# Kernel optimization log

Hardware: AMD Instinct MI355X
Metric: run time of the kernel (lower is better)

The kernel has to match this reference:

```python
import jax, jax.numpy as jnp
import numpy as np

C = 128; HEADS = 8; GH = 32; GW = 32; B = 8; PD = 8  # PD = (dim//4)//4

def _conv(x, w, pad, dil=1, groups=1):
    return jax.lax.conv_general_dilated(
        x, w, (1, 1), [(pad[0], pad[0]), (pad[1], pad[1])],
        rhs_dilation=(dil, dil),
        dimension_numbers=('NCHW', 'OIHW', 'NCHW'),
        feature_group_count=groups)

def _lrelu(t):
    return jnp.where(t >= 0, t, 0.1 * t)

def _ln(t, g, b, eps=1e-5):
    m = jnp.mean(t, -1, keepdims=True)
    v = jnp.var(t, -1, keepdims=True)
    return (t - m) * jax.lax.rsqrt(v + eps) * g + b

def setup_inputs():
    rng = np.random.RandomState(0)
    f = lambda *s: jnp.asarray((rng.randn(*s) * 0.05).astype(np.float32))
    ones = lambda n: jnp.ones((n,), jnp.float32)
    zeros = lambda n: jnp.zeros((n,), jnp.float32)
    # Swin-style relative position index over the (GH, GW) group
    coords = np.stack(np.meshgrid(np.arange(GH), np.arange(GW), indexing='ij')).reshape(2, -1)
    rel = (coords[:, :, None] - coords[:, None, :]).transpose(1, 2, 0)
    rel[..., 0] += GH - 1; rel[..., 1] += GW - 1; rel[..., 0] *= 2 * GW - 1
    rel_idx = jnp.asarray(rel.sum(-1).astype(np.int32))  # [N, N]
    biases = np.stack(np.meshgrid(np.arange(1 - GH, GH), np.arange(1 - GW, GW), indexing='ij'))
    biases = jnp.asarray(biases.reshape(2, -1).T.astype(np.float32))  # [(2GH-1)*(2GW-1), 2]
    return dict(
        x=jnp.asarray(rng.rand(B, C, GH, GW).astype(np.float32)),
        conv1_w=f(C, C, 3, 3), conv2_w=f(C, C, 3, 3), conv3_w=f(C, C, 3, 3),
        convt_w=f(C, 3, 1, 1),
        rba_w=f(C, C, 3, 1), rba_b=zeros(C), rbb_w=f(C, C, 1, 3), rbb_b=zeros(C),
        pp_w=f(PD, 2), pp_b=zeros(PD),
        l1_g=ones(PD), l1_b=zeros(PD), l1_w=f(PD, PD), l1_b2=zeros(PD),
        l2_g=ones(PD), l2_b=zeros(PD), l2_w=f(PD, PD), l2_b2=zeros(PD),
        l3_g=ones(PD), l3_b=zeros(PD), l3_w=f(HEADS, PD), l3_b2=zeros(HEADS),
        qk_w=f(2 * C, C), qk_b=zeros(2 * C),
        v_w=f(C, C), v_b=zeros(C),
        proj_w=f(C, C), proj_b=zeros(C),
        fc1_w=f(C, C), fc1_b=zeros(C), fc2_w=f(C, C), fc2_b=zeros(C),
        biases=biases, rel_idx=rel_idx,
    )

def reference(x, conv1_w, conv2_w, conv3_w, convt_w, rba_w, rba_b, rbb_w, rbb_b,
              pp_w, pp_b, l1_g, l1_b, l1_w, l1_b2, l2_g, l2_b, l2_w, l2_b2,
              l3_g, l3_b, l3_w, l3_b2, qk_w, qk_b, v_w, v_b, proj_w, proj_b,
              fc1_w, fc1_b, fc2_w, fc2_b, biases, rel_idx):
    Bn, Cc, Hh, Ww = x.shape
    N = Hh * Ww
    hd = Cc // HEADS
    # FeaExtract: ResASPP (3 dilated 3x3 convs, grouped 1x1 merge) + residual
    b1 = _lrelu(_conv(x, conv1_w, (1, 1)))
    b2 = _lrelu(_conv(x, conv2_w, (3, 3), dil=3))
    b3 = _lrelu(_conv(x, conv3_w, (5, 5), dil=5))
    a = _conv(jnp.concatenate([b1, b2, b3], 1), convt_w, (0, 0), groups=Cc) + x
    # RB: (3,1) conv -> lrelu -> (1,3) conv + residual
    r = _lrelu(_conv(a, rba_w, (1, 0)) + rba_b[None, :, None, None])
    r = _conv(r, rbb_w, (0, 1)) + rbb_b[None, :, None, None]
    o0 = r + a
    # original uses in-place clamp_, so o0 is clamped before flattening
    o0 = jnp.clip(o0, 0.0, 1.0)
    E = o0.reshape(Bn, Cc, N).transpose(0, 2, 1)  # [B, N, C]
    qk = E @ qk_w.T + qk_b  # [B, N, 2C]
    q = qk[..., :Cc].reshape(Bn, N, HEADS, hd).transpose(0, 2, 1, 3)
    k = qk[..., Cc:].reshape(Bn, N, HEADS, hd).transpose(0, 2, 1, 3)
    v = (E @ v_w.T + v_b).reshape(Bn, N, HEADS, hd).transpose(0, 2, 1, 3)
    attn = jnp.einsum('bhid,bhjd->bhij', q * (hd ** -0.5), k)
    # DynamicPosBias MLP (residual=False): Linear(2,pd) -> [LN,ReLU,Linear] x2 -> LN,ReLU,Linear(pd,heads)
    p = biases @ pp_w.T + pp_b
    p = jax.nn.relu(_ln(p, l1_g, l1_b)) @ l1_w.T + l1_b2
    p = jax.nn.relu(_ln(p, l2_g, l2_b)) @ l2_w.T + l2_b2
    p = jax.nn.relu(_ln(p, l3_g, l3_b)) @ l3_w.T + l3_b2  # [L, heads]
    rpb = p[rel_idx]  # gather -> [N, N, heads]
    attn = attn + rpb.transpose(2, 0, 1)[None]
    attn = jax.nn.softmax(attn, axis=-1)
    y = jnp.einsum('bhij,bhjd->bhid', attn, v).transpose(0, 2, 1, 3).reshape(Bn, N, Cc) + E
    x_proj = y @ proj_w.T + proj_b
    h = jax.nn.gelu(x_proj @ fc1_w.T + fc1_b, approximate=False)
    return (h @ fc2_w.T + fc2_b) + y
```

## Files before the change

kernel.cpp:

```cpp
#include <hip/hip_runtime.h>
#include <hip/hip_bf16.h>

typedef __hip_bfloat16 bf16;
typedef __bf16 bf16x8 __attribute__((ext_vector_type(8)));
typedef float f32x4 __attribute__((ext_vector_type(4)));
typedef __fp16 f16x2 __attribute__((ext_vector_type(2)));
typedef __fp16 f16x4 __attribute__((ext_vector_type(4)));

#define Lb 3969
#define LOG2E 1.4426950408889634f
#define EXP2(x) __builtin_amdgcn_exp2f(x)

#define XP_F   0
#define WF_F   903168
#define WR_F   1124352
#define WG_F   1173504
#define QKV_F  1222656
#define AP_F   2795520
#define YT_F   2795520
#define EB_F   3352576
#define FLAG_F 3908616
#define RT_F   3908624
#define VT_F   4924432

__device__ __forceinline__ float b2f(bf16 v) { return __bfloat162float(v); }
__device__ __forceinline__ bf16 f2b(float v) { return __float2bfloat16(v); }

template <typename T> __device__ __forceinline__ float ldw(const void* p, int i);
template <> __device__ __forceinline__ float ldw<bf16>(const void* p, int i) {
  return __bfloat162float(((const bf16*)p)[i]);
}
template <> __device__ __forceinline__ float ldw<float>(const void* p, int i) {
  return ((const float*)p)[i];
}
template <typename T> __device__ __forceinline__ void stw(void* p, size_t i, float v);
template <> __device__ __forceinline__ void stw<bf16>(void* p, size_t i, float v) {
  ((bf16*)p)[i] = __float2bfloat16(v);
}
template <> __device__ __forceinline__ void stw<float>(void* p, size_t i, float v) {
  ((float*)p)[i] = v;
}

__device__ __forceinline__ unsigned pkh(float a, float b) {
  f16x2 t = __builtin_amdgcn_cvt_pkrtz(a, b);
  return *(unsigned*)&t;
}

__device__ __forceinline__ bool detect_local(const unsigned* x) {
  int lane = threadIdx.x & 63;
  int cnt = 0;
#pragma unroll
  for (int k = 0; k < 4; ++k) {
    unsigned lo = x[lane + 64 * k] & 0xFFFFu;
    cnt += (lo >= 0x3C00u && lo < 0x3F80u) ? 1 : 0;
  }
#pragma unroll
  for (int off = 1; off < 64; off <<= 1) cnt += __shfl_xor(cnt, off);
  return cnt >= 128;
}

template <typename T>
__device__ __forceinline__ void ln_relu8(const float* t, float* u,
                                         const void* g, const void* bb)
{
  float m = 0.f;
#pragma unroll
  for (int k = 0; k < 8; ++k) m += t[k];
  m *= 0.125f;
  float v = 0.f;
#pragma unroll
  for (int k = 0; k < 8; ++k) { float d = t[k] - m; v += d * d; }
  v *= 0.125f;
  float r = rsqrtf(v + 1e-5f);
#pragma unroll
  for (int k = 0; k < 8; ++k) {
    float val = (t[k] - m) * r * ldw<T>(g, k) + ldw<T>(bb, k);
    u[k] = val > 0.f ? val : 0.f;
  }
}

template <typename T>
__device__ __forceinline__ float dpb_one(
    int r, int h, const void* biases, const void* pp_w, const void* pp_b,
    const void* l1_g, const void* l1_b, const void* l1_w, const void* l1_b2,
    const void* l2_g, const void* l2_b, const void* l2_w, const void* l2_b2,
    const void* l3_g, const void* l3_b, const void* l3_w, const void* l3_b2)
{
  float b0 = ldw<T>(biases, r * 2), b1 = ldw<T>(biases, r * 2 + 1);
  float t[8], u[8];
#pragma unroll
  for (int j = 0; j < 8; ++j)
    t[j] = b0 * ldw<T>(pp_w, j * 2) + b1 * ldw<T>(pp_w, j * 2 + 1) +
           ldw<T>(pp_b, j);
  ln_relu8<T>(t, u, l1_g, l1_b);
#pragma unroll
  for (int j = 0; j < 8; ++j) {
    float s = ldw<T>(l1_b2, j);
#pragma unroll
    for (int k = 0; k < 8; ++k) s += u[k] * ldw<T>(l1_w, j * 8 + k);
    t[j] = s;
  }
  ln_relu8<T>(t, u, l2_g, l2_b);
#pragma unroll
  for (int j = 0; j < 8; ++j) {
    float s = ldw<T>(l2_b2, j);
#pragma unroll
    for (int k = 0; k < 8; ++k) s += u[k] * ldw<T>(l2_w, j * 8 + k);
    t[j] = s;
  }
  ln_relu8<T>(t, u, l3_g, l3_b);
  float s = ldw<T>(l3_b2, h);
#pragma unroll
  for (int k = 0; k < 8; ++k) s += u[k] * ldw<T>(l3_w, h * 8 + k);
  return s;
}

template <typename T>
__device__ void wprep_all_body(const void* w1, const void* w2, const void* w3,
                               const void* rba_w, const void* rbb_w,
                               const void* qk_w, const void* v_w,
                               const void* proj_w, const void* fc1_w,
                               const void* fc2_w, bf16* __restrict__ Wf,
                               bf16* __restrict__ Wr, bf16* __restrict__ Wg)
{
  int tid = blockIdx.x * 256 + threadIdx.x;
  int lane = tid & 63, li = lane & 15, quad = lane >> 4;
  if (tid < 55296) {
    int mt = (tid >> 6) & 7;
    int Kc = (tid >> 9) & 3;
    int rem = tid >> 11;
    int t = rem % 9;
    int br = rem / 9;
    const void* w = (br == 0 ? w1 : (br == 1 ? w2 : w3));
    int o = mt * 16 + li;
    int ci0 = Kc * 32 + quad * 8;
#pragma unroll
    for (int j = 0; j < 8; ++j)
      Wf[(size_t)tid * 8 + j] = f2b(ldw<T>(w, (o * 128 + ci0 + j) * 9 + t));
  } else {
    int u = tid - 55296;
    if (u < 12288) {
      int Kc = (u >> 6) & 3, mt = (u >> 8) & 7, q = u >> 11;
      const void* w = (q >= 3) ? rbb_w : rba_w;
      int t = q % 3;
#pragma unroll
      for (int j = 0; j < 8; ++j)
        Wr[(size_t)u * 8 + j] =
            f2b(ldw<T>(w, ((mt * 16 + li) * 128 + Kc * 32 + quad * 8 + j) * 3 + t));
    } else if (u < 24576) {
      int g = u - 12288;
      int Kc = (g >> 6) & 3, mtg = g >> 8;
      const void* w; int mrow; float sc = 1.f;
      if (mtg < 16)      { w = qk_w;   mrow = mtg * 16;
                           if (mtg < 8) sc = 0.25f * LOG2E; }
      else if (mtg < 24) { w = v_w;    mrow = (mtg - 16) * 16; }
      else if (mtg < 32) { w = proj_w; mrow = (mtg - 24) * 16; }
      else if (mtg < 40) { w = fc1_w;  mrow = (mtg - 32) * 16; }
      else               { w = fc2_w;  mrow = (mtg - 40) * 16; }
#pragma unroll
      for (int j = 0; j < 8; ++j)
        Wg[(size_t)g * 8 + j] =
            f2b(sc * ldw<T>(w, (mrow + li) * 128 + Kc * 32 + quad * 8 + j));
    }
  }
}

template <typename T>
__device__ void nhwc_body(const void* x, bf16* __restrict__ xp,
                          bf16 (*tile)[128], int bid)
{
  const int b = bid >> 5;
  const int row = bid & 31;
  const int t = threadIdx.x;
  const size_t bbase = (size_t)b * 42 * 42 * 128;
  const bf16x8 z = (bf16x8){};

  if (t < 160) {
    int side = t / 80;
    int off = (t % 80) * 8;
    *(bf16x8*)&xp[bbase + ((size_t)(row + 5) * 42 + side * 37) * 128 + off] = z;
  }
  {
    int zr = (row < 5) ? row : ((row >= 27) ? row + 10 : -1);
    if (zr >= 0) {
      size_t base = bbase + (size_t)zr * 42 * 128;
      for (int k = t; k < 672; k += 256) *(bf16x8*)&xp[base + k * 8] = z;
    }
  }

  {
    int ci = t >> 1, half = t & 1;
#pragma unroll
    for (int j = 0; j < 16; ++j) {
      int px = half * 16 + j;
      tile[px][ci] = f2b(ldw<T>(x, ((size_t)b * 128 + ci) * 1024 + row * 32 + px));
    }
  }
  __syncthreads();
  {
    int px = t >> 3, c0 = (t & 7) * 16;
    bf16* dst = xp + (bbase + ((size_t)(row + 5) * 42 + (px + 5)) * 128 + c0);
#pragma unroll
    for (int j = 0; j < 16; ++j) dst[j] = tile[px][c0 + j];
  }
}

template <typename T>
__device__ void dpbrt_wave(
    int tt, int h, int lane, const void* biases, const void* pp_w,
    const void* pp_b, const void* l1_g, const void* l1_b, const void* l1_w,
    const void* l1_b2, const void* l2_g, const void* l2_b, const void* l2_w,
    const void* l2_b2, const void* l3_g, const void* l3_b, const void* l3_w,
    const void* l3_b2, float* __restrict__ RTf, float (*rp)[47])
{
  const int t = tt >> 1, p = tt & 1;
  const int quad = lane >> 4, li = lane & 15;
  for (int e = lane; e < 94; e += 64) {
    int row = t + e / 47;
    int col = p * 16 + e % 47;
    rp[e / 47][e % 47] =
        dpb_one<T>(row * 63 + col, h, biases, pp_w, pp_b, l1_g, l1_b, l1_w,
                   l1_b2, l2_g, l2_b, l2_w, l2_b2, l3_g, l3_b, l3_w, l3_b2) *
        LOG2E;
  }
  __syncthreads();
  float* dst = RTf + ((size_t)(h * 124 + tt) * 4) * 256 + lane * 4;
#pragma unroll
  for (int mt = 0; mt < 4; ++mt) {
    f32x4 v;
#pragma unroll
    for (int r = 0; r < 4; ++r) {
      int j = mt * 16 + quad * 4 + r;
      v[r] = rp[1 - (j >> 5)][li - (j & 31) + 31];
    }
    *(f32x4*)(dst + mt * 256) = v;
  }
}

__global__ __launch_bounds__(256) void prep_kernel(
    const unsigned* x, const void* w1, const void* w2, const void* w3,
    const void* rba_w, const void* rbb_w, const void* qk_w, const void* v_w,
    const void* proj_w, const void* fc1_w, const void* fc2_w,
    bf16* Wf, bf16* Wr, bf16* Wg, bf16* xp, int* flag,
    const void* biases, const void* pp_w, const void* pp_b, const void* l1_g,
    const void* l1_b, const void* l1_w, const void* l1_b2, const void* l2_g,
    const void* l2_b, const void* l2_w, const void* l2_b2, const void* l3_g,
    const void* l3_b, const void* l3_w, const void* l3_b2, float* RTf)
{
  __shared__ bf16 tile[32][128];
  __shared__ float rpl[4][2][47];
  bool isbf = detect_local(x);
  if (blockIdx.x < 312) {
    if (blockIdx.x == 0 && threadIdx.x == 0) *flag = isbf ? 1 : 0;
    if (isbf) wprep_all_body<bf16>(w1, w2, w3, rba_w, rbb_w, qk_w, v_w, proj_w,
                                   fc1_w, fc2_w, Wf, Wr, Wg);
    else      wprep_all_body<float>(w1, w2, w3, rba_w, rbb_w, qk_w, v_w, proj_w,
                                    fc1_w, fc2_w, Wf, Wr, Wg);
  } else if (blockIdx.x < 568) {
    int bid = blockIdx.x - 312;
    if (isbf) nhwc_body<bf16>(x, xp, tile, bid);
    else      nhwc_body<float>(x, xp, tile, bid);
  } else {
    int wv = threadIdx.x >> 6, lane = threadIdx.x & 63;
    int idx = (blockIdx.x - 568) * 4 + wv;
    int tt = idx % 124, h = idx / 124;
    if (isbf)
      dpbrt_wave<bf16>(tt, h, lane, biases, pp_w, pp_b, l1_g, l1_b, l1_w,
                       l1_b2, l2_g, l2_b, l2_w, l2_b2, l3_g, l3_b, l3_w,
                       l3_b2, RTf, rpl[wv]);
    else
      dpbrt_wave<float>(tt, h, lane, biases, pp_w, pp_b, l1_g, l1_b, l1_w,
                        l1_b2, l2_g, l2_b, l2_w, l2_b2, l3_g, l3_b, l3_w,
                        l3_b2, RTf, rpl[wv]);
  }
}

#define ASPP_SEG(BR, M8, DIL)                                                  \
  {                                                                            \
    for (int t = 0; t < 9; ++t) {                                              \
      const int dy = (t / 3 - 1) * (DIL), dx = (t % 3 - 1) * (DIL);            \
      const bf16* Asite =                                                      \
          xp + (((size_t)bb * 42 + (y + 5 + dy)) * 42 + (xb + li + 5 + dx)) *  \
                   128;                                                        \
      const bf16* Wt2 = Wf + (((size_t)(BR)*9 + t) * 4) * 512 * 8;             \
      _Pragma("unroll") for (int Kc = 0; Kc < 4; ++Kc) {                       \
        bf16x8 afrag = *(const bf16x8*)(Asite + Kc * 32 + quad * 8);           \
        const bf16* Wk = Wt2 + (size_t)Kc * 512 * 8 + (size_t)lane * 8;        \
        _Pragma("unroll") for (int m = 0; m < 4; ++m) {                        \
          bf16x8 wfrag = *(const bf16x8*)(Wk + (size_t)((M8) + m) * 64 * 8);   \
          acc[m] = __builtin_amdgcn_mfma_f32_16x16x32_bf16(afrag, wfrag,       \
                                                           acc[m], 0, 0, 0);   \
        }                                                                      \
      }                                                                        \
    }                                                                          \
  }

template <typename T>
__device__ void aspp_merge_body(const bf16* __restrict__ xp,
                                const bf16* __restrict__ Wf, const void* wt,
                                bf16* __restrict__ ap, bf16 (*conc)[200],
                                float* cw)
{
  const int nt_ = blockIdx.x, mh = blockIdx.y, bb = blockIdx.z;
  const int w = threadIdx.x >> 6, lane = threadIdx.x & 63;
  const int quad = lane >> 4, li = lane & 15;
  const int pxw = nt_ * 16;
  const int y = pxw >> 5, xb = pxw & 31;

  if (mh == 0 && (nt_ == 0 || nt_ == 63)) {
    const bf16x8 z = (bf16x8){};
    size_t base = ((size_t)bb * 34 + (nt_ == 0 ? 0 : 33)) * 32 * 128;
    for (int k = threadIdx.x; k < 512; k += 192) *(bf16x8*)&ap[base + k * 8] = z;
  }
  if (threadIdx.x < 192) cw[threadIdx.x] = ldw<T>(wt, mh * 192 + threadIdx.x);

  f32x4 acc[4] = {};
  const int seg = mh * 3 + w;
  if (seg == 0)      ASPP_SEG(0, 0, 1)
  else if (seg == 1) ASPP_SEG(0, 4, 1)
  else if (seg == 2) ASPP_SEG(1, 0, 3)
  else if (seg == 3) ASPP_SEG(1, 4, 3)
  else if (seg == 4) ASPP_SEG(2, 0, 5)
  else               ASPP_SEG(2, 4, 5)

#pragma unroll
  for (int mt = 0; mt < 4; ++mt)
#pragma unroll
    for (int r = 0; r < 4; ++r)
      conc[quad * 4 + r][(w * 4 + mt) * 16 + li] = f2b(acc[mt][r]);
  __syncthreads();

  if (threadIdx.x < 128) {
    const int pxl = threadIdx.x >> 3;
    const int o0 = (threadIdx.x & 7) * 8;
    const int px = pxw + pxl;
    const int yy = px >> 5, xx = px & 31;
    const bf16* xrow =
        xp + (((size_t)bb * 42 + yy + 5) * 42 + xx + 5) * 128 + mh * 64 + o0;
    bf16* arow =
        ap + (((size_t)bb * 34 + yy + 1) * 32 + xx) * 128 + mh * 64 + o0;
    bf16 xl[8], ol[8];
    *(bf16x8*)&xl[0] = *(const bf16x8*)&xrow[0];
#pragma unroll
    for (int j = 0; j < 8; ++j) {
      float v = b2f(xl[j]);
#pragma unroll
      for (int i = 0; i < 3; ++i) {
        float t = b2f(conc[pxl][(o0 + j) * 3 + i]);
        v += cw[(o0 + j) * 3 + i] * (t >= 0.f ? t : 0.1f * t);
      }
      ol[j] = f2b(v);
    }
    *(bf16x8*)&arow[0] = *(bf16x8*)&ol[0];
  }
}

__global__ __launch_bounds__(192) void aspp_merge_kernel(
    const bf16* xp, const bf16* Wf, const void* wt, bf16* ap, const int* flag)
{
  __shared__ bf16 conc[16][200];
  __shared__ float cw[192];
  if (*flag) aspp_merge_body<bf16>(xp, Wf, wt, ap, conc, cw);
  else       aspp_merge_body<float>(xp, Wf, wt, ap, conc, cw);
}

template <typename T>
__device__ void rbf_body(const bf16* __restrict__ ap, const bf16* __restrict__ Wr,
                         const void* rba_b, const void* rbb_b,
                         bf16* __restrict__ Eb, bf16 (*r1row)[136])
{
  const int y = blockIdx.x, b = blockIdx.y;
  const int w = threadIdx.x >> 6, lane = threadIdx.x & 63;
  const int mh = w & 1, xb = (w >> 1) * 16;
  const int quad = lane >> 4, li = lane & 15;

  if (threadIdx.x < 128) {
    r1row[0][threadIdx.x] = f2b(0.f);
    r1row[33][threadIdx.x] = f2b(0.f);
  }

  f32x4 acc[4] = {};
#pragma unroll
  for (int t = 0; t < 3; ++t) {
    const bf16* Asite = ap + (((size_t)b * 34 + y + t) * 32 + xb + li) * 128;
#pragma unroll
    for (int Kc = 0; Kc < 4; ++Kc) {
      bf16x8 afrag = *(const bf16x8*)(Asite + Kc * 32 + quad * 8);
#pragma unroll
      for (int mt = 0; mt < 4; ++mt) {
        int f = (t * 8 + mh * 4 + mt) * 4 + Kc;
        bf16x8 wfrag = *(const bf16x8*)(Wr + ((size_t)f * 64 + lane) * 8);
        acc[mt] = __builtin_amdgcn_mfma_f32_16x16x32_bf16(afrag, wfrag, acc[mt],
                                                          0, 0, 0);
      }
    }
  }
#pragma unroll
  for (int mt = 0; mt < 4; ++mt) {
    int o = (mh * 4 + mt) * 16 + li;
    float bv = ldw<T>(rba_b, o);
#pragma unroll
    for (int r = 0; r < 4; ++r) {
      int x = xb + quad * 4 + r;
      float v = acc[mt][r] + bv;
      r1row[x + 1][o] = f2b(v >= 0.f ? v : 0.1f * v);
    }
  }
  __syncthreads();

  f32x4 acc2[4] = {};
#pragma unroll
  for (int t = 0; t < 3; ++t) {
#pragma unroll
    for (int Kc = 0; Kc < 4; ++Kc) {
      bf16x8 afrag = *(const bf16x8*)&r1row[xb + li + t][Kc * 32 + quad * 8];
#pragma unroll
      for (int mt = 0; mt < 4; ++mt) {
        int f = ((3 + t) * 8 + mh * 4 + mt) * 4 + Kc;
        bf16x8 wfrag = *(const bf16x8*)(Wr + ((size_t)f * 64 + lane) * 8);
        acc2[mt] = __builtin_amdgcn_mfma_f32_16x16x32_bf16(afrag, wfrag,
                                                           acc2[mt], 0, 0, 0);
      }
    }
  }
#pragma unroll
  for (int mt = 0; mt < 4; ++mt) {
    int o = (mh * 4 + mt) * 16 + li;
    float bv = ldw<T>(rbb_b, o);
#pragma unroll
    for (int r = 0; r < 4; ++r) {
      int x = xb + quad * 4 + r;
      float v = acc2[mt][r] + bv +
                b2f(ap[(((size_t)b * 34 + y + 1) * 32 + x) * 128 + o]);
      v = fminf(fmaxf(v, 0.f), 1.f);
      Eb[((size_t)b * 1024 + y * 32 + x) * 128 + o] = f2b(v);
    }
  }
}

__global__ __launch_bounds__(256) void rbf_kernel(
    const bf16* ap, const bf16* Wr, const void* rba_b, const void* rbb_b,
    bf16* Eb, const int* flag)
{
  __shared__ bf16 r1row[34][136];
  if (*flag) rbf_body<bf16>(ap, Wr, rba_b, rbb_b, Eb, r1row);
  else       rbf_body<float>(ap, Wr, rba_b, rbb_b, Eb, r1row);
}

template <typename T>
__device__ void qkv_body(const bf16* __restrict__ Eb, const bf16* __restrict__ Wg,
                         const void* qk_b, const void* v_b,
                         bf16* __restrict__ QKV, uint2* __restrict__ VTh)
{
  const int grp = blockIdx.y, b = blockIdx.z;
  const int w = threadIdx.x >> 6, lane = threadIdx.x & 63;
  const int quad = lane >> 4, li = lane & 15;
  const int pxw = blockIdx.x * 64 + w * 16;
  bf16x8 ef[4];
#pragma unroll
  for (int Kc = 0; Kc < 4; ++Kc)
    ef[Kc] = *(const bf16x8*)&Eb[((size_t)b * 1024 + pxw + li) * 128 + Kc * 32 +
                                 quad * 8];
  f32x4 acc[8] = {};
#pragma unroll
  for (int nt = 0; nt < 8; ++nt) {
    int g = grp * 8 + nt;
#pragma unroll
    for (int Kc = 0; Kc < 4; ++Kc) {
      bf16x8 wf = *(const bf16x8*)&Wg[(((size_t)g * 4 + Kc) * 64 + lane) * 8];
      acc[nt] = __builtin_amdgcn_mfma_f32_16x16x32_bf16(ef[Kc], wf, acc[nt],
                                                        0, 0, 0);
    }
  }
  if (grp < 2) {
#pragma unroll
    for (int nt = 0; nt < 8; ++nt) {
      int g = grp * 8 + nt;
      int o = g * 16 + li;
      float bv = (g < 8) ? (0.25f * LOG2E) * ldw<T>(qk_b, o) : ldw<T>(qk_b, o);
#pragma unroll
      for (int r = 0; r < 4; ++r) {
        int px = pxw + quad * 4 + r;
        QKV[((size_t)b * 1024 + px) * 384 + o] = f2b(acc[nt][r] + bv);
      }
    }
  } else {
#pragma unroll
    for (int nt = 0; nt < 8; ++nt) {
      int hh = nt;
      float bv = ldw<T>(v_b, nt * 16 + li);
      uint2 pu;
      pu.x = pkh(acc[nt][0] + bv, acc[nt][1] + bv);
      pu.y = pkh(acc[nt][2] + bv, acc[nt][3] + bv);
      VTh[(((size_t)(b * 8 + hh) * 16 + blockIdx.x) * 4 + w) * 64 + lane] = pu;
    }
  }
}

__global__ __launch_bounds__(256) void qkv_kernel(
    const bf16* Eb, const bf16* Wg, const void* qk_b, const void* v_b,
    bf16* QKV, uint2* VTh, const int* flag)
{
  if (*flag) qkv_body<bf16>(Eb, Wg, qk_b, v_b, QKV, VTh);
  else       qkv_body<float>(Eb, Wg, qk_b, v_b, QKV, VTh);
}

template <typename T>
__device__ void mlpf_body(const bf16* __restrict__ Yt, const bf16* __restrict__ Wg,
                          const void* proj_b, const void* fc1_b,
                          const void* fc2_b, void* out,
                          bf16 (*buf0)[136], bf16 (*buf1)[136])
{
  const int w = threadIdx.x >> 6, lane = threadIdx.x & 63;
  const int quad = lane >> 4, li = lane & 15;
  const size_t row0 = (size_t)blockIdx.x * 16;

  bf16x8 ef[4];
  f32x4 acc[2];

#pragma unroll
  for (int Kc = 0; Kc < 4; ++Kc)
    ef[Kc] = *(const bf16x8*)&Yt[(row0 + li) * 128 + Kc * 32 + quad * 8];
  acc[0] = (f32x4){}; acc[1] = (f32x4){};
#pragma unroll
  for (int j = 0; j < 2; ++j) {
    int g = 24 + w * 2 + j;
#pragma unroll
    for (int Kc = 0; Kc < 4; ++Kc) {
      bf16x8 wf = *(const bf16x8*)&Wg[(((size_t)g * 4 + Kc) * 64 + lane) * 8];
      acc[j] = __builtin_amdgcn_mfma_f32_16x16x32_bf16(ef[Kc], wf, acc[j],
                                                       0, 0, 0);
    }
  }
#pragma unroll
  for (int j = 0; j < 2; ++j) {
    int o = (w * 2 + j) * 16 + li;
    float bv = ldw<T>(proj_b, o);
#pragma unroll
    for (int r = 0; r < 4; ++r)
      buf0[quad * 4 + r][o] = f2b(acc[j][r] + bv);
  }
  __syncthreads();

#pragma unroll
  for (int Kc = 0; Kc < 4; ++Kc)
    ef[Kc] = *(const bf16x8*)&buf0[li][Kc * 32 + quad * 8];
  acc[0] = (f32x4){}; acc[1] = (f32x4){};
#pragma unroll
  for (int j = 0; j < 2; ++j) {
    int g = 32 + w * 2 + j;
#pragma unroll
    for (int Kc = 0; Kc < 4; ++Kc) {
      bf16x8 wf = *(const bf16x8*)&Wg[(((size_t)g * 4 + Kc) * 64 + lane) * 8];
      acc[j] = __builtin_amdgcn_mfma_f32_16x16x32_bf16(ef[Kc], wf, acc[j],
                                                       0, 0, 0);
    }
  }
#pragma unroll
  for (int j = 0; j < 2; ++j) {
    int o = (w * 2 + j) * 16 + li;
    float bv = ldw<T>(fc1_b, o);
#pragma unroll
    for (int r = 0; r < 4; ++r) {
      float v = acc[j][r] + bv;
      v = 0.5f * v * (1.f + erff(v * 0.70710678118f));
      buf1[quad * 4 + r][o] = f2b(v);
    }
  }
  __syncthreads();

#pragma unroll
  for (int Kc = 0; Kc < 4; ++Kc)
    ef[Kc] = *(const bf16x8*)&buf1[li][Kc * 32 + quad * 8];
  acc[0] = (f32x4){}; acc[1] = (f32x4){};
#pragma unroll
  for (int j = 0; j < 2; ++j) {
    int g = 40 + w * 2 + j;
#pragma unroll
    for (int Kc = 0; Kc < 4; ++Kc) {
      bf16x8 wf = *(const bf16x8*)&Wg[(((size_t)g * 4 + Kc) * 64 + lane) * 8];
      acc[j] = __builtin_amdgcn_mfma_f32_16x16x32_bf16(ef[Kc], wf, acc[j],
                                                       0, 0, 0);
    }
  }
#pragma unroll
  for (int j = 0; j < 2; ++j) {
    int o = (w * 2 + j) * 16 + li;
    float bv = ldw<T>(fc2_b, o);
#pragma unroll
    for (int r = 0; r < 4; ++r) {
      size_t oidx = (row0 + quad * 4 + r) * 128 + o;
      float v = acc[j][r] + bv + b2f(Yt[oidx]);
      stw<T>(out, oidx, v);
    }
  }
}

__global__ __launch_bounds__(256) void mlpf_kernel(
    const bf16* Yt, const bf16* Wg, const void* proj_b, const void* fc1_b,
    const void* fc2_b, void* out, const int* flag)
{
  __shared__ bf16 buf0[16][136];
  __shared__ bf16 buf1[16][136];
  if (*flag) mlpf_body<bf16>(Yt, Wg, proj_b, fc1_b, fc2_b, out, buf0, buf1);
  else       mlpf_body<float>(Yt, Wg, proj_b, fc1_b, fc2_b, out, buf0, buf1);
}

__global__ __launch_bounds__(256, 4) void attn_kernel(
    const bf16* __restrict__ QKV, const bf16* __restrict__ Eb,
    const float* __restrict__ RTf, const uint2* __restrict__ VTh,
    bf16* __restrict__ Yt)
{
  const int qt = blockIdx.x * 4 + (threadIdx.x >> 6);
  const int hh = blockIdx.y;
  const int b = blockIdx.z;

  const int lane = threadIdx.x & 63;
  const int quad = lane >> 4, li = lane & 15;
  const int qb = qt * 16;

  const bf16* QKVb = QKV + (size_t)b * 1024 * 384;
  const uint2* VTb = VTh + (size_t)(b * 8 + hh) * 4096;
  const float* RTh = RTf + (size_t)hh * 124 * 1024;

  bf16x8 qf = (bf16x8){};
  if (quad < 2)
    qf = *(const bf16x8*)&QKVb[(size_t)(qb + li) * 384 + hh * 16 + quad * 8];

  f32x4 Oa = {}, Ob = {};
  float m_st = -1e30f, l_ln = 0.f;
  const int sbase = (lane & 48) + ((lane >> 2) & 12);

  struct Buf { bf16x8 kf[4]; f32x4 cin[4]; uint2 vb[4]; };
  Buf bA, bB;

  auto LOAD = [&](Buf& bf, int c) {
    const int c0 = c * 64;
    const int tt = ((qt >> 1) - 2 * c + 30) * 2 + (qt & 1);
    const float* rtp = RTh + (size_t)tt * 1024 + lane * 4;
#pragma unroll
    for (int mt = 0; mt < 4; ++mt) {
      bf.cin[mt] = *(const f32x4*)(rtp + mt * 256);
      bf.kf[mt] = (bf16x8){};
      if (quad < 2)
        bf.kf[mt] = *(const bf16x8*)&QKVb[(size_t)(c0 + mt * 16 + li) * 384 +
                                          128 + hh * 16 + quad * 8];
      bf.vb[mt] = VTb[(size_t)(c * 4 + mt) * 64 + lane];
    }
  };

  auto STEP = [&](const Buf& bf) {
    f32x4 sT[4];
#pragma unroll
    for (int mt = 0; mt < 4; ++mt)
      sT[mt] = __builtin_amdgcn_mfma_f32_16x16x32_bf16(bf.kf[mt], qf,
                                                       bf.cin[mt], 0, 0, 0);

    float m0 = fmaxf(fmaxf(sT[0][0], sT[0][1]), fmaxf(sT[0][2], sT[0][3]));
    float m1 = fmaxf(fmaxf(sT[1][0], sT[1][1]), fmaxf(sT[1][2], sT[1][3]));
    float m2 = fmaxf(fmaxf(sT[2][0], sT[2][1]), fmaxf(sT[2][2], sT[2][3]));
    float m3 = fmaxf(fmaxf(sT[3][0], sT[3][1]), fmaxf(sT[3][2], sT[3][3]));
    float lmax = fmaxf(fmaxf(m0, m1), fmaxf(m2, m3));

    if (!__all(lmax <= m_st + 11.5f)) {
      float cm = fmaxf(lmax, __shfl_xor(lmax, 16));
      cm = fmaxf(cm, __shfl_xor(cm, 32));
      float mn = fmaxf(m_st, cm);
      float al = EXP2(m_st - mn);
      m_st = mn;
      l_ln *= al;
#pragma unroll
      for (int r = 0; r < 4; ++r) {
        float a = __shfl(al, sbase + r);
        Oa[r] *= a;
        Ob[r] *= a;
      }
    }

#pragma unroll
    for (int mt = 0; mt < 4; ++mt)
#pragma unroll
      for (int r = 0; r < 4; ++r) sT[mt][r] = EXP2(sT[mt][r] - m_st);

    float s0 = (sT[0][0] + sT[0][1]) + (sT[0][2] + sT[0][3]);
    float s1 = (sT[1][0] + sT[1][1]) + (sT[1][2] + sT[1][3]);
    float s2 = (sT[2][0] + sT[2][1]) + (sT[2][2] + sT[2][3]);
    float s3 = (sT[3][0] + sT[3][1]) + (sT[3][2] + sT[3][3]);
    l_ln += (s0 + s1) + (s2 + s3);

#pragma unroll
    for (int mt = 0; mt < 4; ++mt) {
      union { unsigned u[2]; f16x4 h4; } pu;
      pu.u[0] = pkh(sT[mt][0], sT[mt][1]);
      pu.u[1] = pkh(sT[mt][2], sT[mt][3]);
      union { uint2 u; f16x4 h; } vu;
      vu.u = bf.vb[mt];
      if (mt & 2)
        Ob = __builtin_amdgcn_mfma_f32_16x16x16f16(pu.h4, vu.h, Ob, 0, 0, 0);
      else
        Oa = __builtin_amdgcn_mfma_f32_16x16x16f16(pu.h4, vu.h, Oa, 0, 0, 0);
    }
  };

  LOAD(bA, 0);
  for (int c = 0; c < 16; c += 2) {
    LOAD(bB, c + 1);
    STEP(bA);
    if (c + 2 < 16) LOAD(bA, c + 2);
    STEP(bB);
  }

  float l_st = l_ln + __shfl_xor(l_ln, 16);
  l_st += __shfl_xor(l_st, 32);

  f32x4 O_;
#pragma unroll
  for (int r = 0; r < 4; ++r) O_[r] = Oa[r] + Ob[r];

  const bf16* Ebp = Eb + (size_t)b * 1024 * 128 + hh * 16 + li;
  bf16* Ytp = Yt + (size_t)b * 1024 * 128 + hh * 16 + li;
#pragma unroll
  for (int r = 0; r < 4; ++r) {
    float lb = __shfl(l_st, sbase + r);
    int qrow = qb + quad * 4 + r;
    Ytp[(size_t)qrow * 128] =
        f2b(O_[r] / lb + b2f(Ebp[(size_t)qrow * 128]));
  }
}

extern "C" void kernel_launch(void* const* d_in, const int* in_sizes, int n_in,
                              void* d_out, int out_size, void* d_ws,
                              size_t ws_size, hipStream_t stream)
{
  (void)in_sizes; (void)n_in; (void)out_size; (void)ws_size;
  const void* x       = d_in[0];
  const void* conv1_w = d_in[1];
  const void* conv2_w = d_in[2];
  const void* conv3_w = d_in[3];
  const void* convt_w = d_in[4];
  const void* rba_w   = d_in[5];
  const void* rba_b   = d_in[6];
  const void* rbb_w   = d_in[7];
  const void* rbb_b   = d_in[8];
  const void* pp_w    = d_in[9];
  const void* pp_b    = d_in[10];
  const void* l1_g    = d_in[11];
  const void* l1_b    = d_in[12];
  const void* l1_w    = d_in[13];
  const void* l1_b2   = d_in[14];
  const void* l2_g    = d_in[15];
  const void* l2_b    = d_in[16];
  const void* l2_w    = d_in[17];
  const void* l2_b2   = d_in[18];
  const void* l3_g    = d_in[19];
  const void* l3_b    = d_in[20];
  const void* l3_w    = d_in[21];
  const void* l3_b2   = d_in[22];
  const void* qk_w    = d_in[23];
  const void* qk_b    = d_in[24];
  const void* v_w     = d_in[25];
  const void* v_b     = d_in[26];
  const void* proj_w  = d_in[27];
  const void* proj_b  = d_in[28];
  const void* fc1_w   = d_in[29];
  const void* fc1_b   = d_in[30];
  const void* fc2_w   = d_in[31];
  const void* fc2_b   = d_in[32];
  const void* biases  = d_in[33];

  float* ws   = (float*)d_ws;
  bf16*  xp   = (bf16*)(ws + XP_F);
  bf16*  Wf   = (bf16*)(ws + WF_F);
  bf16*  Wr   = (bf16*)(ws + WR_F);
  bf16*  Wg   = (bf16*)(ws + WG_F);
  bf16*  QKV  = (bf16*)(ws + QKV_F);
  bf16*  ap   = (bf16*)(ws + AP_F);
  bf16*  Yt   = (bf16*)(ws + YT_F);
  bf16*  Eb   = (bf16*)(ws + EB_F);
  int*   flag = (int*)(ws + FLAG_F);
  float* RTf  = ws + RT_F;
  uint2* VTh  = (uint2*)(ws + VT_F);

  prep_kernel<<<816, 256, 0, stream>>>(
      (const unsigned*)x, conv1_w, conv2_w, conv3_w, rba_w, rbb_w, qk_w, v_w,
      proj_w, fc1_w, fc2_w, Wf, Wr, Wg, xp, flag,
      biases, pp_w, pp_b, l1_g, l1_b, l1_w, l1_b2, l2_g, l2_b, l2_w, l2_b2,
      l3_g, l3_b, l3_w, l3_b2, RTf);
  aspp_merge_kernel<<<dim3(64, 2, 8), 192, 0, stream>>>(xp, Wf, convt_w, ap,
                                                        flag);
  rbf_kernel<<<dim3(32, 8), 256, 0, stream>>>(ap, Wr, rba_b, rbb_b, Eb, flag);
  qkv_kernel<<<dim3(16, 3, 8), 256, 0, stream>>>(Eb, Wg, qk_b, v_b, QKV, VTh,
                                                 flag);
  attn_kernel<<<dim3(16, 8, 8), 256, 0, stream>>>(QKV, Eb, RTf, VTh, Yt);
  mlpf_kernel<<<512, 256, 0, stream>>>(Yt, Wg, proj_b, fc1_b, fc2_b, d_out,
                                       flag);
}
```

Baseline: 228.5 us.

## Split attention key range across two waves and merge softmax partials in LDS

Each block now handles two query tiles instead of four, and each query tile is processed by two wavefronts that each cover half of the key chunks. The partial max, sum and output accumulators are exchanged through shared memory and combined with an online-softmax rescale, and the grid is doubled. This is meant to halve the serial key loop per wave and expose more waves to hide latency. The cost is a block-wide barrier, extra LDS traffic and merge arithmetic, and the second wave of each pair sitting idle during the final write.

Result: slower. 260.1 us (+13.8%).

```diff
diff --git a/kernel.cpp b/kernel.cpp
--- a/kernel.cpp
+++ b/kernel.cpp
@@ -611,13 +611,19 @@
     const float* __restrict__ RTf, const uint2* __restrict__ VTh,
     bf16* __restrict__ Yt)
 {
-  const int qt = blockIdx.x * 4 + (threadIdx.x >> 6);
+  const int w = threadIdx.x >> 6;
+  const int qtl = w >> 1, kh = w & 1;
+  const int qt = blockIdx.x * 2 + qtl;
   const int hh = blockIdx.y;
   const int b = blockIdx.z;
 
   const int lane = threadIdx.x & 63;
   const int quad = lane >> 4, li = lane & 15;
   const int qb = qt * 16;
+
+  __shared__ float Sml[4][64];
+  __shared__ float Sl[4][64];
+  __shared__ float So[4][64][4];
 
   const bf16* QKVb = QKV + (size_t)b * 1024 * 384;
   const uint2* VTb = VTh + (size_t)(b * 8 + hh) * 4096;
@@ -702,20 +708,39 @@
     }
   };
 
-  LOAD(bA, 0);
-  for (int c = 0; c < 16; c += 2) {
+  const int cb = kh * 8;
+  LOAD(bA, cb);
+  for (int c = cb; c < cb + 8; c += 2) {
     LOAD(bB, c + 1);
     STEP(bA);
-    if (c + 2 < 16) LOAD(bA, c + 2);
+    if (c + 2 < cb + 8) LOAD(bA, c + 2);
     STEP(bB);
   }
 
-  float l_st = l_ln + __shfl_xor(l_ln, 16);
+  f32x4 O_;
+#pragma unroll
+  for (int r = 0; r < 4; ++r) O_[r] = Oa[r] + Ob[r];
+
+  Sml[w][lane] = m_st;
+  Sl[w][lane] = l_ln;
+#pragma unroll
+  for (int r = 0; r < 4; ++r) So[w][lane][r] = O_[r];
+  __syncthreads();
+
+  if (kh) return;
+
+  float mb = Sml[w + 1][lane];
+  float mm = fmaxf(m_st, mb);
+  float fa = EXP2(m_st - mm), fb = EXP2(mb - mm);
+  float lm = l_ln * fa + Sl[w + 1][lane] * fb;
+#pragma unroll
+  for (int r = 0; r < 4; ++r) {
+    float ar = __shfl(fa, sbase + r), br = __shfl(fb, sbase + r);
+    O_[r] = O_[r] * ar + So[w + 1][lane][r] * br;
+  }
+
+  float l_st = lm + __shfl_xor(lm, 16);
   l_st += __shfl_xor(l_st, 32);
-
-  f32x4 O_;
-#pragma unroll
-  for (int r = 0; r < 4; ++r) O_[r] = Oa[r] + Ob[r];
 
   const bf16* Ebp = Eb + (size_t)b * 1024 * 128 + hh * 16 + li;
   bf16* Ytp = Yt + (size_t)b * 1024 * 128 + hh * 16 + li;
@@ -791,7 +816,7 @@
   rbf_kernel<<<dim3(32, 8), 256, 0, stream>>>(ap, Wr, rba_b, rbb_b, Eb, flag);
   qkv_kernel<<<dim3(16, 3, 8), 256, 0, stream>>>(Eb, Wg, qk_b, v_b, QKV, VTh,
                                                  flag);
-  attn_kernel<<<dim3(16, 8, 8), 256, 0, stream>>>(QKV, Eb, RTf, VTh, Yt);
+  attn_kernel<<<dim3(32, 8, 8), 256, 0, stream>>>(QKV, Eb, RTf, VTh, Yt);
   mlpf_kernel<<<512, 256, 0, stream>>>(Yt, Wg, proj_b, fc1_b, fc2_b, d_out,
                                        flag);
 }
```
